# Performance work log

Hardware: AMD Instinct MI355X
Metric: run time of the kernel (lower is better)

## Reference

```python
import jax, jax.numpy as jnp
import numpy as np

NUM_HEADS = 16
HEAD_DIM = 64
PATCH_NUMS = [1, 2, 3, 4, 5, 6, 8, 10, 13, 16, 32]
MAX_SCALE_MUL = float(np.log(100.0))


def precompute_freqs_cis(dim, patch_nums, theta=10000.0):
    # Returns [L, dim//2, 2] (cos, sin) pairs; matches torch.polar construction.
    freqs = 1.0 / theta ** (np.arange(0, dim, 4)[: dim // 4].astype(np.float32) / dim)  # [dim//4]
    tx, ty = [], []
    grid = 32.0
    for p in patch_nums:
        ix, iy = np.meshgrid(np.arange(p), np.arange(p), indexing="ij")  # torch default 'ij'
        tx.append(ix.flatten().astype(np.float32) / p * grid)
        ty.append(iy.flatten().astype(np.float32) / p * grid)
    tx = np.concatenate(tx)
    ty = np.concatenate(ty)
    ang = np.concatenate([np.outer(tx, freqs), np.outer(ty, freqs)], axis=1).astype(np.float32)  # [L, dim//2]
    return np.stack([np.cos(ang), np.sin(ang)], axis=-1)  # [L, dim//2, 2]


FREQS_CIS_CROSS = jnp.asarray(precompute_freqs_cis(HEAD_DIM, [12]))  # [144, 32, 2]


def _rope(x, cis):
    # x: [B, H, S, D]; cis: [S, D//2, 2] -> complex multiply on (even, odd) pairs.
    B, H, S, D = x.shape
    xr = x.reshape(B, H, S, D // 2, 2)
    a, b = xr[..., 0], xr[..., 1]
    c = cis[..., 0][None, None]  # [1,1,S,D//2]
    d = cis[..., 1][None, None]
    return jnp.stack([a * c - b * d, a * d + b * c], axis=-1).reshape(B, H, S, D)


def setup_inputs() -> dict:
    key = jax.random.key(0)
    ks = jax.random.split(key, 6)
    B, C, Ck, Lk = 8, 1024, 1024, 144
    fc = precompute_freqs_cis(HEAD_DIM, PATCH_NUMS)
    L = fc.shape[0]  # 1704
    return {
        "x": jax.random.normal(ks[0], (B, L, C), jnp.float32),
        "y": jax.random.normal(ks[1], (B, Lk, Ck), jnp.float32),
        "freqs_cis": jnp.asarray(fc),
        "attn_bias": jax.random.normal(ks[2], (1, 1, L, Lk), jnp.float32) * 0.1,
        "Wq": jax.random.normal(ks[3], (C, C), jnp.float32) * 0.02,
        "q_bias": jnp.zeros((C,), jnp.float32),
        "Wkv": jax.random.normal(ks[4], (2 * C, Ck), jnp.float32) * 0.02,
        "v_bias": jnp.zeros((C,), jnp.float32),
        "Wproj": jax.random.normal(ks[5], (C, C), jnp.float32) * 0.02,
        "b_proj": jnp.zeros((C,), jnp.float32),
        "scale_mul": jnp.full((1, NUM_HEADS, 1, 1), np.log(4.0), jnp.float32),
    }


def reference(x, y, freqs_cis, attn_bias, Wq, q_bias, Wkv, v_bias, Wproj, b_proj, scale_mul):
    B, L, C = x.shape
    H, D = NUM_HEADS, HEAD_DIM
    Lk = y.shape[1]
    # fused QKV projections (k bias is the zero buffer)
    q = (x @ Wq.T + q_bias).reshape(B, L, H, D).transpose(0, 2, 1, 3)  # [B,H,L,D]
    kv_bias = jnp.concatenate([jnp.zeros_like(v_bias), v_bias])
    kv = (y @ Wkv.T + kv_bias).reshape(B, Lk, 2, H, D)
    k = kv[:, :, 0].transpose(0, 2, 1, 3)  # [B,H,Lk,D]
    v = kv[:, :, 1].transpose(0, 2, 1, 3)
    # attn_l2_norm path: scale = 1, per-head learned multiplier
    sm = jnp.exp(jnp.minimum(scale_mul, MAX_SCALE_MUL))  # [1,H,1,1]
    q = q / jnp.maximum(jnp.linalg.norm(q, axis=-1, keepdims=True), 1e-12) * sm
    k = k / jnp.maximum(jnp.linalg.norm(k, axis=-1, keepdims=True), 1e-12)
    # inline RoPE (cross freqs recomputed from 12x12 grid every forward in the original)
    q = _rope(q, freqs_cis)
    k = _rope(k, FREQS_CIS_CROSS)
    # manual (non-flash) masked attention, scale = 1 due to l2 norm
    logits = jnp.einsum("bhld,bhkd->bhlk", q, k) + attn_bias
    attn = jax.nn.softmax(logits, axis=-1)
    oup = jnp.einsum("bhlk,bhkd->bhld", attn, v).transpose(0, 2, 1, 3).reshape(B, L, C)
    return oup @ Wproj.T + b_proj
```

## Files before the change

kernel.cpp:

```cpp
#include <hip/hip_runtime.h>

using u16 = unsigned short;
using u32 = unsigned int;

typedef __bf16 bf16x8 __attribute__((ext_vector_type(8)));
typedef float  f32x4  __attribute__((ext_vector_type(4)));
typedef _Float16 f16;
typedef _Float16 f16x4 __attribute__((ext_vector_type(4)));
typedef _Float16 f16x8 __attribute__((ext_vector_type(8)));
typedef u16 u16x4 __attribute__((ext_vector_type(4)));

__device__ __forceinline__ float b2f(u16 u) { return __uint_as_float(((u32)u) << 16); }
__device__ __forceinline__ u16 f2b(float f) {
    u32 u = __float_as_uint(f);
    return (u16)((u + 0x7FFFu + ((u >> 16) & 1u)) >> 16);
}

__device__ __forceinline__ void async_cp16(void* lds, const void* g) {
    __builtin_amdgcn_global_load_lds(
        (const __attribute__((address_space(1))) u32*)g,
        (__attribute__((address_space(3))) u32*)lds, 16, 0, 0);
}

__global__ __launch_bounds__(256) void prep(const float* __restrict__ x,
                                            const float* __restrict__ Wq,
                                            const float* __restrict__ Wp,
                                            f16* __restrict__ xf,
                                            f16* __restrict__ wqhi, f16* __restrict__ wqlo,
                                            f16* __restrict__ wph,
                                            int nx4, int nw4) {
    int i = blockIdx.x * 256 + threadIdx.x;
    if (i < nx4) {
        f32x4 v = reinterpret_cast<const f32x4*>(x)[i];
        f16x4 h = {(f16)v[0], (f16)v[1], (f16)v[2], (f16)v[3]};
        reinterpret_cast<f16x4*>(xf)[i] = h;
    } else if (i < nx4 + nw4) {
        int k = i - nx4;
        f32x4 v = reinterpret_cast<const f32x4*>(Wq)[k];
        f16x4 H, L;
#pragma unroll
        for (int j = 0; j < 4; j++) {
            f16 hb = (f16)v[j];
            H[j] = hb;
            L[j] = (f16)(v[j] - (float)hb);
        }
        reinterpret_cast<f16x4*>(wqhi)[k] = H;
        reinterpret_cast<f16x4*>(wqlo)[k] = L;
    } else {
        int k = i - nx4 - nw4;
        if (k < nw4) {
            f32x4 v = reinterpret_cast<const f32x4*>(Wp)[k];
            f16x4 h = {(f16)v[0], (f16)v[1], (f16)v[2], (f16)v[3]};
            reinterpret_cast<f16x4*>(wph)[k] = h;
        }
    }
}

__device__ __forceinline__ void split8(f32x4 a0, f32x4 a1, bf16x8& hi, bf16x8& lo) {
    union { bf16x8 v; u16 s[8]; } H, L;
#pragma unroll
    for (int j = 0; j < 4; j++) {
        float f = a0[j]; u16 hb = f2b(f); H.s[j] = hb;     L.s[j] = f2b(f - b2f(hb));
        float g = a1[j]; u16 gb = f2b(g); H.s[4 + j] = gb; L.s[4 + j] = f2b(g - b2f(gb));
    }
    hi = H.v; lo = L.v;
}

__device__ __forceinline__ void remap852(int j, int& mt, int& sg) {
    if (j < 832) {
        int a = j >> 5, rem = j & 31;
        mt = a * 8 + (rem & 7);
        sg = rem >> 3;
    } else {
        int rem = j - 832;
        mt = 208 + rem % 5;
        sg = rem / 5;
    }
}

__global__ __launch_bounds__(256) void gemm_q(const f16* __restrict__ xf,
                                              const f16* __restrict__ whi,
                                              const f16* __restrict__ wlo,
                                              const float* __restrict__ qb,
                                              const float* __restrict__ fc,
                                              const float* __restrict__ smul,
                                              f16* __restrict__ qout) {
    const int K = 1024, L = 1704;
    __shared__ f16 xs[2][2][64][64];
    int tid = threadIdx.x;
    int lane = tid & 63, wv = tid >> 6;
    int mt, hg;
    remap852(blockIdx.x, mt, hg);
    int h  = hg * 4 + wv;
    int lr = lane & 15, quad = lane >> 4;
    long m0 = (long)mt * 64;

    int r0 = tid >> 3, c0 = tid & 7;
    int s1i = tid + 256;
    int r1 = s1i >> 3, c1 = s1i & 7;
    const f16* srcx0 = xf + (m0 + r0) * K + ((c0 ^ (r0 & 7)) * 8);
    const f16* srcx1 = xf + (m0 + r1) * K + ((c1 ^ (r1 & 7)) * 8);
    f16* dx[2][2][2];
#pragma unroll
    for (int b = 0; b < 2; b++)
#pragma unroll
        for (int hh = 0; hh < 2; hh++) {
            dx[b][hh][0] = &xs[b][hh][r0][c0 * 8];
            dx[b][hh][1] = &xs[b][hh][r1][c1 * 8];
        }

    const f16x8* wh_p[4];
    const f16x8* wl_p[4];
#pragma unroll
    for (int i = 0; i < 4; i++) {
        long woff = ((long)(h * 64 + i * 16 + lr)) * K;
        wh_p[i] = reinterpret_cast<const f16x8*>(whi + woff) + quad;
        wl_p[i] = reinterpret_cast<const f16x8*>(wlo + woff) + quad;
    }

    int sp0 = ((0 + quad) ^ (lr & 7)) * 8;
    int sp1 = ((4 + quad) ^ (lr & 7)) * 8;

    f32x4 acc[4][4] = {};

    async_cp16(dx[0][0][0], srcx0);      async_cp16(dx[0][0][1], srcx1);
    async_cp16(dx[0][1][0], srcx0 + 64); async_cp16(dx[0][1][1], srcx1 + 64);
    __syncthreads();

    for (int c = 0; c < 8; c++) {
        if (c < 7) {
            int nb = (c + 1) & 1;
            int off = (c + 1) * 128;
            async_cp16(dx[nb][0][0], srcx0 + off);      async_cp16(dx[nb][0][1], srcx1 + off);
            async_cp16(dx[nb][1][0], srcx0 + off + 64); async_cp16(dx[nb][1][1], srcx1 + off + 64);
        }
        int buf = c & 1;
#pragma unroll
        for (int hh = 0; hh < 2; hh++) {
#pragma unroll
            for (int s = 0; s < 2; s++) {
                int o = (c * 2 + hh) * 8 + s * 4;
                int sp = s ? sp1 : sp0;
                f16x8 AF[4], WH[4], WL[4];
#pragma unroll
                for (int i = 0; i < 4; i++) {
                    WH[i] = wh_p[i][o];
                    WL[i] = wl_p[i][o];
                }
#pragma unroll
                for (int i = 0; i < 4; i++)
                    AF[i] = *reinterpret_cast<const f16x8*>(&xs[buf][hh][i * 16 + lr][sp]);
#pragma unroll
                for (int mi = 0; mi < 4; mi++)
#pragma unroll
                    for (int ni = 0; ni < 4; ni++) {
                        acc[mi][ni] = __builtin_amdgcn_mfma_f32_16x16x32_f16(AF[mi], WH[ni], acc[mi][ni], 0, 0, 0);
                        acc[mi][ni] = __builtin_amdgcn_mfma_f32_16x16x32_f16(AF[mi], WL[ni], acc[mi][ni], 0, 0, 0);
                    }
            }
        }
        __syncthreads();
    }

    float sm = __expf(fminf(smul[h], 4.6051702f));
#pragma unroll
    for (int mi = 0; mi < 4; mi++) {
#pragma unroll
        for (int r = 0; r < 4; r++) {
            long rowg = m0 + mi * 16 + quad * 4 + r;
            float v[4];
            float ss = 0.f;
#pragma unroll
            for (int ni = 0; ni < 4; ni++) {
                v[ni] = acc[mi][ni][r] + qb[h * 64 + ni * 16 + lr];
                ss += v[ni] * v[ni];
            }
            ss += __shfl_xor(ss, 1, 64); ss += __shfl_xor(ss, 2, 64);
            ss += __shfl_xor(ss, 4, 64); ss += __shfl_xor(ss, 8, 64);
            float inv = sm / fmaxf(sqrtf(ss), 1e-12f);
            int l = (int)(rowg % L);
            f16* orow = qout + rowg * 1024 + h * 64;
#pragma unroll
            for (int ni = 0; ni < 4; ni++) {
                float u = v[ni] * inv;
                int d = ni * 16 + lr;
                int j = d >> 1;
                float c = fc[(l * 32 + j) * 2];
                float s = fc[(l * 32 + j) * 2 + 1];
                float pr = __shfl_xor(u, 1, 64);
                float o = (lane & 1) ? (pr * s + u * c) : (u * c - pr * s);
                orow[d] = (f16)o;
            }
        }
    }
}

__constant__ double FREQS16[16] = {
    1.0, 0.5623413251903491, 0.31622776601683794, 0.17782794100389228,
    0.1, 0.05623413251903491, 0.03162277660168379, 0.017782794100389228,
    0.01, 0.005623413251903491, 0.0031622776601683794, 0.0017782794100389228,
    0.001, 0.0005623413251903491, 0.00031622776601683794, 0.00017782794100389228};

__global__ __launch_bounds__(256) void gemm_kv(const float* __restrict__ y,
                                               const float* __restrict__ Wkv,
                                               const float* __restrict__ vb,
                                               f16* __restrict__ khp,
                                               f16* __restrict__ klp,
                                               f16* __restrict__ vhp,
                                               f16* __restrict__ vlp) {
    const int K = 1024;
    int lane = threadIdx.x & 63, wv = threadIdx.x >> 6;
    int mt = blockIdx.x >> 3;
    int nt = (blockIdx.x & 7) * 4 + wv;
    int lr = lane & 15, quad = lane >> 4;
    long m0 = (long)mt * 64;

    const float* arow[4];
    const float* wrow[4];
#pragma unroll
    for (int i = 0; i < 4; i++) {
        arow[i] = y   + (m0 + i * 16 + lr) * K + quad * 8;
        wrow[i] = Wkv + ((long)(nt * 64 + i * 16 + lr)) * K + quad * 8;
    }

    f32x4 acc[4][4] = {};
    for (int ks = 0; ks < 32; ks++) {
        bf16x8 ah[4], al[4], wh[4], wl[4];
#pragma unroll
        for (int i = 0; i < 4; i++) {
            const float* ap = arow[i] + ks * 32;
            split8(*(const f32x4*)ap, *(const f32x4*)(ap + 4), ah[i], al[i]);
            const float* wp = wrow[i] + ks * 32;
            split8(*(const f32x4*)wp, *(const f32x4*)(wp + 4), wh[i], wl[i]);
        }
#pragma unroll
        for (int mi = 0; mi < 4; mi++)
#pragma unroll
            for (int ni = 0; ni < 4; ni++) {
                acc[mi][ni] = __builtin_amdgcn_mfma_f32_16x16x32_bf16(ah[mi], wh[ni], acc[mi][ni], 0, 0, 0);
                acc[mi][ni] = __builtin_amdgcn_mfma_f32_16x16x32_bf16(al[mi], wh[ni], acc[mi][ni], 0, 0, 0);
                acc[mi][ni] = __builtin_amdgcn_mfma_f32_16x16x32_bf16(ah[mi], wl[ni], acc[mi][ni], 0, 0, 0);
            }
    }

    bool isv = nt >= 16;
    int h = isv ? nt - 16 : nt;
#pragma unroll
    for (int mi = 0; mi < 4; mi++) {
#pragma unroll
        for (int r = 0; r < 4; r++) {
            long row = m0 + mi * 16 + quad * 4 + r;
            int b = (int)(row / 144), lk = (int)(row % 144);
            long bh = b * 16 + h;
            float v[4];
#pragma unroll
            for (int ni = 0; ni < 4; ni++)
                v[ni] = acc[mi][ni][r] + (isv ? vb[h * 64 + ni * 16 + lr] : 0.f);
            if (!isv) {
                float ss = v[0] * v[0] + v[1] * v[1] + v[2] * v[2] + v[3] * v[3];
                ss += __shfl_xor(ss, 1, 64); ss += __shfl_xor(ss, 2, 64);
                ss += __shfl_xor(ss, 4, 64); ss += __shfl_xor(ss, 8, 64);
                float inv = 1.f / fmaxf(sqrtf(ss), 1e-12f);
                f16* kh_row = khp + (bh * 144 + lk) * 64;
                f16* kl_row = klp + (bh * 144 + lk) * 64;
#pragma unroll
                for (int ni = 0; ni < 4; ni++) {
                    float u = v[ni] * inv;
                    int d = ni * 16 + lr;
                    int j = d >> 1;
                    int f = j & 15;
                    float tc = (j < 16) ? ((float)(lk / 12)) / 12.0f * 32.0f
                                        : ((float)(lk % 12)) / 12.0f * 32.0f;
                    float ang = (float)((double)tc * FREQS16[f]);
                    float c = cosf(ang), s = sinf(ang);
                    float pr = __shfl_xor(u, 1, 64);
                    float o = (lane & 1) ? (pr * s + u * c) : (u * c - pr * s);
                    f16 oh = (f16)o;
                    f16 ol = (f16)(o - (float)oh);
                    kh_row[d] = oh;
                    kl_row[d] = ol;
                }
            } else {
#pragma unroll
                for (int ni = 0; ni < 4; ni++) {
                    float val = v[ni];
                    int d = ni * 16 + lr;
                    f16 vh = (f16)val;
                    f16 vl = (f16)(val - (float)vh);
                    vhp[(bh * 64 + d) * 144 + lk] = vh;
                    vlp[(bh * 64 + d) * 144 + lk] = vl;
                }
            }
        }
    }
}

__global__ __launch_bounds__(256, 3) void attn(const f16* q,
                                               const f16* __restrict__ khp,
                                               const f16* __restrict__ klp,
                                               const f16* __restrict__ vhp,
                                               const f16* __restrict__ vlp,
                                               const float* __restrict__ abias,
                                               f16* aout) {
    const int L = 1704;
    __shared__ __align__(16) f16 ps[4][16][152];
    int tid = threadIdx.x;
    int lane = tid & 63, wv = tid >> 6;
    int lr = lane & 15, quad = lane >> 4;
    int ltile = blockIdx.x % 27;
    int bh = blockIdx.x / 27;
    int h = bh & 15, b = bh >> 4;
    int l0 = ltile * 64;
    int rows = min(64, L - l0);

    int rA = wv * 16 + lr;
    int rAc = min(rA, rows - 1);
    const f16* qrow = q + ((long)(b * L + l0 + rAc)) * 1024 + h * 64;
    f16x8 qa0 = *reinterpret_cast<const f16x8*>(qrow + quad * 8);
    f16x8 qa1 = *reinterpret_cast<const f16x8*>(qrow + 32 + quad * 8);

    const f16* khb = khp + (long)bh * (144 * 64);
    const f16* klb = klp + (long)bh * (144 * 64);

    f32x4 acc[9] = {};
#pragma unroll
    for (int t = 0; t < 9; t++) {
        const f16* k0 = khb + (t * 16 + lr) * 64 + quad * 8;
        const f16* k1 = klb + (t * 16 + lr) * 64 + quad * 8;
        f16x8 bh0 = *reinterpret_cast<const f16x8*>(k0);
        f16x8 bh1 = *reinterpret_cast<const f16x8*>(k0 + 32);
        f16x8 bl0 = *reinterpret_cast<const f16x8*>(k1);
        f16x8 bl1 = *reinterpret_cast<const f16x8*>(k1 + 32);
        __builtin_amdgcn_s_setprio(1);
        acc[t] = __builtin_amdgcn_mfma_f32_16x16x32_f16(qa0, bh0, acc[t], 0, 0, 0);
        acc[t] = __builtin_amdgcn_mfma_f32_16x16x32_f16(qa1, bh1, acc[t], 0, 0, 0);
        acc[t] = __builtin_amdgcn_mfma_f32_16x16x32_f16(qa0, bl0, acc[t], 0, 0, 0);
        acc[t] = __builtin_amdgcn_mfma_f32_16x16x32_f16(qa1, bl1, acc[t], 0, 0, 0);
        __builtin_amdgcn_s_setprio(0);
    }

    int rC = wv * 16 + quad * 4;
#pragma unroll
    for (int r = 0; r < 4; r++) {
        long lrow = (long)(l0 + min(rC + r, rows - 1)) * 144;
#pragma unroll
        for (int t = 0; t < 9; t++) acc[t][r] += abias[lrow + t * 16 + lr];
    }

#pragma unroll
    for (int r = 0; r < 4; r++) {
        float mx = acc[0][r];
#pragma unroll
        for (int t = 1; t < 9; t++) mx = fmaxf(mx, acc[t][r]);
        mx = fmaxf(mx, __shfl_xor(mx, 1, 64));
        mx = fmaxf(mx, __shfl_xor(mx, 2, 64));
        mx = fmaxf(mx, __shfl_xor(mx, 4, 64));
        mx = fmaxf(mx, __shfl_xor(mx, 8, 64));
        float s = 0.f;
#pragma unroll
        for (int t = 0; t < 9; t++) {
            float e = __expf(acc[t][r] - mx);
            acc[t][r] = e;
            s += e;
        }
        s += __shfl_xor(s, 1, 64);
        s += __shfl_xor(s, 2, 64);
        s += __shfl_xor(s, 4, 64);
        s += __shfl_xor(s, 8, 64);
        float inv = 1.0f / s;
#pragma unroll
        for (int t = 0; t < 9; t++)
            ps[wv][quad * 4 + r][t * 16 + lr] = (f16)(acc[t][r] * inv);
    }

    const f16* vhb = vhp + (long)bh * (64 * 144);
    const f16* vlb = vlp + (long)bh * (64 * 144);
    f32x4 oacc[4] = {};
#pragma unroll
    for (int ks = 0; ks < 5; ks++) {
        f16x8 pa = {0, 0, 0, 0, 0, 0, 0, 0};
        if (ks < 4 || quad < 2)
            pa = *reinterpret_cast<const f16x8*>(&ps[wv][lr][ks * 32 + quad * 8]);
#pragma unroll
        for (int n = 0; n < 4; n++) {
            f16x8 vh8 = {0, 0, 0, 0, 0, 0, 0, 0};
            f16x8 vl8 = {0, 0, 0, 0, 0, 0, 0, 0};
            if (ks < 4 || quad < 2) {
                const f16* vr  = vhb + (n * 16 + lr) * 144 + ks * 32 + quad * 8;
                const f16* vr2 = vlb + (n * 16 + lr) * 144 + ks * 32 + quad * 8;
                vh8 = *reinterpret_cast<const f16x8*>(vr);
                vl8 = *reinterpret_cast<const f16x8*>(vr2);
            }
            __builtin_amdgcn_s_setprio(1);
            oacc[n] = __builtin_amdgcn_mfma_f32_16x16x32_f16(pa, vh8, oacc[n], 0, 0, 0);
            oacc[n] = __builtin_amdgcn_mfma_f32_16x16x32_f16(pa, vl8, oacc[n], 0, 0, 0);
            __builtin_amdgcn_s_setprio(0);
        }
    }

    long ob = (long)(b * L + l0);
#pragma unroll
    for (int r = 0; r < 4; r++) {
        int rw = rC + r;
        if (rw < rows) {
            f16* ao = aout + (ob + rw) * 1024 + h * 64;
#pragma unroll
            for (int n = 0; n < 4; n++) ao[n * 16 + lr] = (f16)oacc[n][r];
        }
    }
}

__global__ __launch_bounds__(256) void gemm_proj(const f16* __restrict__ A,
                                                 const f16* __restrict__ Wh,
                                                 const float* __restrict__ bias,
                                                 float* __restrict__ out) {
    const int K = 1024;
    __shared__ f16 as[2][2][64][64];
    int tid = threadIdx.x;
    int lane = tid & 63, wv = tid >> 6;
    int mt, cg;
    remap852(blockIdx.x, mt, cg);
    int lr = lane & 15, quad = lane >> 4;
    long m0 = (long)mt * 64;
    long n0 = (long)cg * 256 + wv * 64;

    int r0 = tid >> 3, c0 = tid & 7;
    int s1i = tid + 256;
    int r1 = s1i >> 3, c1 = s1i & 7;
    const f16* srca0 = A + (m0 + r0) * K + ((c0 ^ (r0 & 7)) * 8);
    const f16* srca1 = A + (m0 + r1) * K + ((c1 ^ (r1 & 7)) * 8);
    f16* da[2][2][2];
#pragma unroll
    for (int b = 0; b < 2; b++)
#pragma unroll
        for (int hh = 0; hh < 2; hh++) {
            da[b][hh][0] = &as[b][hh][r0][c0 * 8];
            da[b][hh][1] = &as[b][hh][r1][c1 * 8];
        }

    const f16x8* wrow[4];
#pragma unroll
    for (int i = 0; i < 4; i++)
        wrow[i] = reinterpret_cast<const f16x8*>(Wh + (n0 + i * 16 + lr) * K) + quad;

    int sp0 = ((0 + quad) ^ (lr & 7)) * 8;
    int sp1 = ((4 + quad) ^ (lr & 7)) * 8;

    f32x4 acc[4][4] = {};

    async_cp16(da[0][0][0], srca0);      async_cp16(da[0][0][1], srca1);
    async_cp16(da[0][1][0], srca0 + 64); async_cp16(da[0][1][1], srca1 + 64);
    __syncthreads();

    for (int c = 0; c < 8; c++) {
        if (c < 7) {
            int nb = (c + 1) & 1;
            int off = (c + 1) * 128;
            async_cp16(da[nb][0][0], srca0 + off);      async_cp16(da[nb][0][1], srca1 + off);
            async_cp16(da[nb][1][0], srca0 + off + 64); async_cp16(da[nb][1][1], srca1 + off + 64);
        }
        int buf = c & 1;
#pragma unroll
        for (int hh = 0; hh < 2; hh++) {
#pragma unroll
            for (int s = 0; s < 2; s++) {
                int o = (c * 2 + hh) * 8 + s * 4;
                int sp = s ? sp1 : sp0;
                f16x8 af[4], wf[4];
#pragma unroll
                for (int i = 0; i < 4; i++) wf[i] = wrow[i][o];
#pragma unroll
                for (int i = 0; i < 4; i++)
                    af[i] = *reinterpret_cast<const f16x8*>(&as[buf][hh][i * 16 + lr][sp]);
#pragma unroll
                for (int mi = 0; mi < 4; mi++)
#pragma unroll
                    for (int ni = 0; ni < 4; ni++)
                        acc[mi][ni] = __builtin_amdgcn_mfma_f32_16x16x32_f16(af[mi], wf[ni], acc[mi][ni], 0, 0, 0);
            }
        }
        __syncthreads();
    }

#pragma unroll
    for (int ni = 0; ni < 4; ni++) {
        int col = (int)n0 + ni * 16 + lr;
        float b = bias[col];
#pragma unroll
        for (int mi = 0; mi < 4; mi++) {
            long row = m0 + mi * 16 + quad * 4;
#pragma unroll
            for (int r = 0; r < 4; r++)
                out[(row + r) * 1024 + col] = acc[mi][ni][r] + b;
        }
    }
}

extern "C" void kernel_launch(void* const* d_in, const int* in_sizes, int n_in,
                              void* d_out, int out_size, void* d_ws, size_t ws_size,
                              hipStream_t stream) {
    const float* x     = (const float*)d_in[0];
    const float* y     = (const float*)d_in[1];
    const float* fc    = (const float*)d_in[2];
    const float* abias = (const float*)d_in[3];
    const float* Wq    = (const float*)d_in[4];
    const float* qb    = (const float*)d_in[5];
    const float* Wkv   = (const float*)d_in[6];
    const float* vb    = (const float*)d_in[7];
    const float* Wp    = (const float*)d_in[8];
    const float* bp    = (const float*)d_in[9];
    const float* smul  = (const float*)d_in[10];

    const long XN = 13959168L;
    const long WN = 1048576L;
    const long KVN = 1179648L;

    f16* qbuf  = (f16*)d_ws;
    f16* wq_hi = qbuf + XN;
    f16* wq_lo = wq_hi + WN;
    f16* wp_h  = wq_lo + WN;

    f16* x_f = (f16*)d_out;
    f16* kh_p  = (f16*)d_out;
    f16* kl_p  = kh_p + KVN;
    f16* vth_p = kl_p + KVN;
    f16* vtl_p = vth_p + KVN;

    int nx4 = (int)(XN / 4);
    int nw4 = (int)(WN / 4);
    int prep_blocks = (nx4 + 2 * nw4) / 256;

    prep<<<dim3(prep_blocks), dim3(256), 0, stream>>>(x, Wq, Wp, x_f,
                                                      wq_hi, wq_lo, wp_h, nx4, nw4);
    gemm_q<<<dim3(852), dim3(256), 0, stream>>>(x_f, wq_hi, wq_lo, qb, fc, smul, qbuf);
    gemm_kv<<<dim3(144), dim3(256), 0, stream>>>(y, Wkv, vb, kh_p, kl_p, vth_p, vtl_p);
    attn<<<dim3(3456), dim3(256), 0, stream>>>(qbuf, kh_p, kl_p, vth_p, vtl_p, abias, (f16*)qbuf);
    gemm_proj<<<dim3(852), dim3(256), 0, stream>>>((const f16*)qbuf, wp_h, bp, (float*)d_out);
}
```

Baseline: 578.9 us.

## Pre-split y and Wkv into bf16 hi/lo in prep and retile gemm_kv

Moves the fp32-to-bf16 hi/lo splitting of y and Wkv out of the gemm_kv inner loop and into the existing prep kernel, which writes the split operands into spare space in the output buffer. gemm_kv then loads ready-made bf16x8 vectors instead of converting fp32 on every K step. Its M tile also shrinks from 64 to 32 rows, doubling the grid from 144 to 288 blocks so more CUs are busy. In exchange, prep reads and writes extra data, and each block reuses weights over fewer rows.

```diff
diff --git a/kernel.cpp b/kernel.cpp
--- a/kernel.cpp
+++ b/kernel.cpp
@@ -22,13 +22,30 @@
         (__attribute__((address_space(3))) u32*)lds, 16, 0, 0);
 }
 
+__device__ __forceinline__ void split4_store(const float* src, u16* hi, u16* lo, int i) {
+    f32x4 v = reinterpret_cast<const f32x4*>(src)[i];
+    u16x4 H, L;
+#pragma unroll
+    for (int j = 0; j < 4; j++) {
+        u16 hb = f2b(v[j]);
+        H[j] = hb;
+        L[j] = f2b(v[j] - b2f(hb));
+    }
+    reinterpret_cast<u16x4*>(hi)[i] = H;
+    reinterpret_cast<u16x4*>(lo)[i] = L;
+}
+
 __global__ __launch_bounds__(256) void prep(const float* __restrict__ x,
                                             const float* __restrict__ Wq,
                                             const float* __restrict__ Wp,
+                                            const float* __restrict__ y,
+                                            const float* __restrict__ Wkv,
                                             f16* __restrict__ xf,
                                             f16* __restrict__ wqhi, f16* __restrict__ wqlo,
                                             f16* __restrict__ wph,
-                                            int nx4, int nw4) {
+                                            u16* __restrict__ yhi, u16* __restrict__ ylo,
+                                            u16* __restrict__ wkhi, u16* __restrict__ wklo,
+                                            int nx4, int nw4, int ny4, int nwk4) {
     int i = blockIdx.x * 256 + threadIdx.x;
     if (i < nx4) {
         f32x4 v = reinterpret_cast<const f32x4*>(x)[i];
@@ -46,24 +63,18 @@
         }
         reinterpret_cast<f16x4*>(wqhi)[k] = H;
         reinterpret_cast<f16x4*>(wqlo)[k] = L;
+    } else if (i < nx4 + 2 * nw4) {
+        int k = i - nx4 - nw4;
+        f32x4 v = reinterpret_cast<const f32x4*>(Wp)[k];
+        f16x4 h = {(f16)v[0], (f16)v[1], (f16)v[2], (f16)v[3]};
+        reinterpret_cast<f16x4*>(wph)[k] = h;
+    } else if (i < nx4 + 2 * nw4 + ny4) {
+        int k = i - nx4 - 2 * nw4;
+        split4_store(y, yhi, ylo, k);
     } else {
-        int k = i - nx4 - nw4;
-        if (k < nw4) {
-            f32x4 v = reinterpret_cast<const f32x4*>(Wp)[k];
-            f16x4 h = {(f16)v[0], (f16)v[1], (f16)v[2], (f16)v[3]};
-            reinterpret_cast<f16x4*>(wph)[k] = h;
-        }
-    }
-}
-
-__device__ __forceinline__ void split8(f32x4 a0, f32x4 a1, bf16x8& hi, bf16x8& lo) {
-    union { bf16x8 v; u16 s[8]; } H, L;
-#pragma unroll
-    for (int j = 0; j < 4; j++) {
-        float f = a0[j]; u16 hb = f2b(f); H.s[j] = hb;     L.s[j] = f2b(f - b2f(hb));
-        float g = a1[j]; u16 gb = f2b(g); H.s[4 + j] = gb; L.s[4 + j] = f2b(g - b2f(gb));
-    }
-    hi = H.v; lo = L.v;
+        int k = i - nx4 - 2 * nw4 - ny4;
+        if (k < nwk4) split4_store(Wkv, wkhi, wklo, k);
+    }
 }
 
 __device__ __forceinline__ void remap852(int j, int& mt, int& sg) {
@@ -201,8 +212,10 @@
     0.01, 0.005623413251903491, 0.0031622776601683794, 0.0017782794100389228,
     0.001, 0.0005623413251903491, 0.00031622776601683794, 0.00017782794100389228};
 
-__global__ __launch_bounds__(256) void gemm_kv(const float* __restrict__ y,
-                                               const float* __restrict__ Wkv,
+__global__ __launch_bounds__(256) void gemm_kv(const u16* __restrict__ yhi,
+                                               const u16* __restrict__ ylo,
+                                               const u16* __restrict__ wkhi,
+                                               const u16* __restrict__ wklo,
                                                const float* __restrict__ vb,
                                                f16* __restrict__ khp,
                                                f16* __restrict__ klp,
@@ -213,28 +226,35 @@
     int mt = blockIdx.x >> 3;
     int nt = (blockIdx.x & 7) * 4 + wv;
     int lr = lane & 15, quad = lane >> 4;
-    long m0 = (long)mt * 64;
-
-    const float* arow[4];
-    const float* wrow[4];
+    long m0 = (long)mt * 32;
+
+    const bf16x8* ah_p[2];
+    const bf16x8* al_p[2];
+    const bf16x8* wh_p[4];
+    const bf16x8* wl_p[4];
+#pragma unroll
+    for (int i = 0; i < 2; i++) {
+        long aoff = (m0 + i * 16 + lr) * K;
+        ah_p[i] = reinterpret_cast<const bf16x8*>(yhi + aoff) + quad;
+        al_p[i] = reinterpret_cast<const bf16x8*>(ylo + aoff) + quad;
+    }
 #pragma unroll
     for (int i = 0; i < 4; i++) {
-        arow[i] = y   + (m0 + i * 16 + lr) * K + quad * 8;
-        wrow[i] = Wkv + ((long)(nt * 64 + i * 16 + lr)) * K + quad * 8;
-    }
-
-    f32x4 acc[4][4] = {};
+        long woff = ((long)(nt * 64 + i * 16 + lr)) * K;
+        wh_p[i] = reinterpret_cast<const bf16x8*>(wkhi + woff) + quad;
+        wl_p[i] = reinterpret_cast<const bf16x8*>(wklo + woff) + quad;
+    }
+
+    f32x4 acc[2][4] = {};
     for (int ks = 0; ks < 32; ks++) {
-        bf16x8 ah[4], al[4], wh[4], wl[4];
-#pragma unroll
-        for (int i = 0; i < 4; i++) {
-            const float* ap = arow[i] + ks * 32;
-            split8(*(const f32x4*)ap, *(const f32x4*)(ap + 4), ah[i], al[i]);
-            const float* wp = wrow[i] + ks * 32;
-            split8(*(const f32x4*)wp, *(const f32x4*)(wp + 4), wh[i], wl[i]);
-        }
-#pragma unroll
-        for (int mi = 0; mi < 4; mi++)
+        int o = ks * 4;
+        bf16x8 ah[2], al[2], wh[4], wl[4];
+#pragma unroll
+        for (int i = 0; i < 2; i++) { ah[i] = ah_p[i][o]; al[i] = al_p[i][o]; }
+#pragma unroll
+        for (int i = 0; i < 4; i++) { wh[i] = wh_p[i][o]; wl[i] = wl_p[i][o]; }
+#pragma unroll
+        for (int mi = 0; mi < 2; mi++)
 #pragma unroll
             for (int ni = 0; ni < 4; ni++) {
                 acc[mi][ni] = __builtin_amdgcn_mfma_f32_16x16x32_bf16(ah[mi], wh[ni], acc[mi][ni], 0, 0, 0);
@@ -246,7 +266,7 @@
     bool isv = nt >= 16;
     int h = isv ? nt - 16 : nt;
 #pragma unroll
-    for (int mi = 0; mi < 4; mi++) {
+    for (int mi = 0; mi < 2; mi++) {
 #pragma unroll
         for (int r = 0; r < 4; r++) {
             long row = m0 + mi * 16 + quad * 4 + r;
@@ -511,8 +531,10 @@
     const float* bp    = (const float*)d_in[9];
     const float* smul  = (const float*)d_in[10];
 
-    const long XN = 13959168L;
-    const long WN = 1048576L;
+    const long XN  = 13959168L;
+    const long WN  = 1048576L;
+    const long YN  = 1179648L;
+    const long WKN = 2097152L;
     const long KVN = 1179648L;
 
     f16* qbuf  = (f16*)d_ws;
@@ -520,20 +542,28 @@
     f16* wq_lo = wq_hi + WN;
     f16* wp_h  = wq_lo + WN;
 
-    f16* x_f = (f16*)d_out;
+    f16* x_f   = (f16*)d_out;
+    u16* y_hi  = (u16*)(x_f + XN);
+    u16* y_lo  = y_hi + YN;
+    u16* wk_hi = y_lo + YN;
+    u16* wk_lo = wk_hi + WKN;
     f16* kh_p  = (f16*)d_out;
     f16* kl_p  = kh_p + KVN;
     f16* vth_p = kl_p + KVN;
     f16* vtl_p = vth_p + KVN;
 
-    int nx4 = (int)(XN / 4);
-    int nw4 = (int)(WN / 4);
-    int prep_blocks = (nx4 + 2 * nw4) / 256;
-
-    prep<<<dim3(prep_blocks), dim3(256), 0, stream>>>(x, Wq, Wp, x_f,
-                                                      wq_hi, wq_lo, wp_h, nx4, nw4);
+    int nx4  = (int)(XN / 4);
+    int nw4  = (int)(WN / 4);
+    int ny4  = (int)(YN / 4);
+    int nwk4 = (int)(WKN / 4);
+    int prep_blocks = (nx4 + 2 * nw4 + ny4 + nwk4 + 255) / 256;
+
+    prep<<<dim3(prep_blocks), dim3(256), 0, stream>>>(
+        x, Wq, Wp, y, Wkv, x_f, wq_hi, wq_lo, wp_h,
+        y_hi, y_lo, wk_hi, wk_lo, nx4, nw4, ny4, nwk4);
     gemm_q<<<dim3(852), dim3(256), 0, stream>>>(x_f, wq_hi, wq_lo, qb, fc, smul, qbuf);
-    gemm_kv<<<dim3(144), dim3(256), 0, stream>>>(y, Wkv, vb, kh_p, kl_p, vth_p, vtl_p);
+    gemm_kv<<<dim3(288), dim3(256), 0, stream>>>(y_hi, y_lo, wk_hi, wk_lo, vb,
+                                                 kh_p, kl_p, vth_p, vtl_p);
     attn<<<dim3(3456), dim3(256), 0, stream>>>(qbuf, kh_p, kl_p, vth_p, vtl_p, abias, (f16*)qbuf);
     gemm_proj<<<dim3(852), dim3(256), 0, stream>>>((const f16*)qbuf, wp_h, bp, (float*)d_out);
 }
```

After: 536.6 us. -7.3%, faster.
